# Optimization experiments

Measured on AMD Instinct MI355X. Metric: run time of the kernel, lower is better.

The kernel has to match this reference:

```python
import jax, jax.numpy as jnp
import numpy as np
import math

B, T, C = 2, 2048, 2048
NH, L = 16, 128  # n_head, LCompression


def setup_inputs() -> dict:
    key = jax.random.key(0)
    ks = jax.random.split(key, 7)
    s = 0.02
    return {
        "x": jax.random.normal(ks[0], (B, T, C), dtype=jnp.float32),
        # latent: Linear(n_embd -> LComp), stored as [in, out]
        "W_lat": jax.random.normal(ks[1], (C, L), dtype=jnp.float32) * s,
        "b_lat": jnp.zeros((L,), dtype=jnp.float32),
        # Wd: Linear(n_embd -> n_head*LComp)
        "W_d": jax.random.normal(ks[2], (C, NH * L), dtype=jnp.float32) * s,
        "b_d": jnp.zeros((NH * L,), dtype=jnp.float32),
        # c_proj: Linear(n_head*LComp -> n_embd)
        "W_proj": jax.random.normal(ks[3], (NH * L, C), dtype=jnp.float32) * s,
        "b_proj": jnp.zeros((C,), dtype=jnp.float32),
    }


def reference(x, W_lat, b_lat, W_d, b_d, W_proj, b_proj):
    Bx, Tx, Cx = x.shape
    # shared low-rank latent, used as both K and V (identical across heads)
    k = x @ W_lat + b_lat                                   # [B,T,L]
    q = (x @ W_d + b_d).reshape(Bx, Tx, NH, L)              # [B,T,H,L]
    q = jnp.transpose(q, (0, 2, 1, 3))                      # [B,H,T,L]
    scale = 1.0 / math.sqrt(L)
    # scores against the head-shared latent (no per-head K expansion)
    att = jnp.einsum("bhtl,bsl->bhts", q, k) * scale        # [B,H,T,T]
    causal = jnp.tril(jnp.ones((Tx, Tx), dtype=bool))
    att = jnp.where(causal[None, None], att, -jnp.inf)
    att = jax.nn.softmax(att, axis=-1)
    y = jnp.einsum("bhts,bsl->bhtl", att, k)                # [B,H,T,L]
    y = jnp.transpose(y, (0, 2, 1, 3)).reshape(Bx, Tx, NH * L)
    return y @ W_proj + b_proj                              # [B,T,C]
```

## Files before the change

### kernel.cpp

```cpp
#include <hip/hip_runtime.h>
#include <hip/hip_bf16.h>

#define B_   2
#define T_   2048
#define C_   2048
#define NH_  16
#define L_   128
#define NKQ  2176
#define MTOK 4096
#define SCALE2_ 0.12753785792696073f

typedef short short8 __attribute__((ext_vector_type(8)));
typedef float f32x4  __attribute__((ext_vector_type(4)));
typedef float f32x16 __attribute__((ext_vector_type(16)));

#define GLD16(gp, lp) __builtin_amdgcn_global_load_lds(                      \
    (const __attribute__((address_space(1))) void*)(gp),                     \
    (__attribute__((address_space(3))) void*)(lp), 16, 0, 0)

__device__ __forceinline__ unsigned short f2bf(float f) {
  union { float f; unsigned u; } x; x.f = f;
  unsigned r = x.u + 0x7fffu + ((x.u >> 16) & 1u);
  return (unsigned short)(r >> 16);
}

__global__ __launch_bounds__(256) void prep_all(
    const float* __restrict__ x, const float* __restrict__ W_lat,
    const float* __restrict__ W_d, const float* __restrict__ W_proj,
    const float* __restrict__ b_lat, const float* __restrict__ b_d,
    unsigned short* __restrict__ x_bf, unsigned short* __restrict__ BtCat,
    unsigned short* __restrict__ WprojT, float* __restrict__ biascat) {
  __shared__ float tile[32][33];
  int bid = blockIdx.x;
  const int tid = threadIdx.x;

  if (bid < 8192) {
    int i = bid * 1024 + tid * 4;
    float4 v = *(const float4*)(x + i);
    ushort4 o;
    o.x = f2bf(v.x); o.y = f2bf(v.y); o.z = f2bf(v.z); o.w = f2bf(v.w);
    *(ushort4*)(x_bf + i) = o;
    return;
  }
  bid -= 8192;

  const float* W; unsigned short* Wt; int K, N; float mul; int nbx;
  if (bid < 256) {
    W = W_lat; Wt = BtCat; K = C_; N = L_; mul = 1.f; nbx = 4;
  } else if (bid < 256 + 4096) {
    bid -= 256;
    W = W_d; Wt = BtCat + (size_t)L_ * C_; K = C_; N = NH_ * L_; mul = SCALE2_; nbx = 64;
  } else if (bid < 256 + 8192) {
    bid -= 256 + 4096;
    W = W_proj; Wt = WprojT; K = NH_ * L_; N = C_; mul = 1.f; nbx = 64;
  } else {
    int i = (bid - (256 + 8192)) * 256 + tid;
    if (i < L_) biascat[i] = b_lat[i];
    else if (i < NKQ) biascat[i] = b_d[i - L_] * SCALE2_;
    return;
  }

  const int bx = (bid % nbx) * 32, by = (bid / nbx) * 32;
  const int tx = tid & 31, ty = tid >> 5;
  #pragma unroll
  for (int i2 = 0; i2 < 4; i2++)
    tile[ty + i2 * 8][tx] = W[(size_t)(by + ty + i2 * 8) * N + bx + tx];
  __syncthreads();
  #pragma unroll
  for (int i2 = 0; i2 < 4; i2++)
    Wt[(size_t)(bx + ty + i2 * 8) * K + by + tx] = f2bf(tile[tx][ty + i2 * 8] * mul);
}

__global__ void transpose_lat(const unsigned short* __restrict__ kq,
                              unsigned short* __restrict__ KlT) {
  __shared__ unsigned short tile[32][33];
  int t0 = blockIdx.x * 32, l0 = blockIdx.y * 32, b = blockIdx.z;
  int tx = threadIdx.x, ty = threadIdx.y;
  #pragma unroll
  for (int i = 0; i < 4; i++)
    tile[ty + i * 8][tx] = kq[((size_t)b * T_ + t0 + ty + i * 8) * NKQ + l0 + tx];
  __syncthreads();
  #pragma unroll
  for (int i = 0; i < 4; i++)
    KlT[((size_t)b * L_ + l0 + ty + i * 8) * T_ + t0 + tx] = tile[tx][ty + i * 8];
}

__global__ __launch_bounds__(256) void gemm_bt_bias(
    const unsigned short* __restrict__ A,
    const unsigned short* __restrict__ Bt,
    const float* __restrict__ bias,
    unsigned short* __restrict__ Cb,
    float* __restrict__ Cf,
    int M, int N, int K) {
  __shared__ __align__(16) unsigned short As[2][128 * 32];
  __shared__ __align__(16) unsigned short Bs[2][128 * 32];
  const int tid  = threadIdx.x;
  const int wave = tid >> 6, lane = tid & 63;
  const int lcol = lane & 15, quad = lane >> 4;
  const int m0 = blockIdx.x * 128, n0 = blockIdx.y * 128;
  const int wm = (wave >> 1) * 64, wn = (wave & 1) * 64;
  const int lrow = lane >> 2, lchunk = (lane & 3) * 8;
  const int rb = wave * 32;

  f32x4 acc[4][4];
  #pragma unroll
  for (int i = 0; i < 4; i++)
    #pragma unroll
    for (int j = 0; j < 4; j++) acc[i][j] = (f32x4){0.f, 0.f, 0.f, 0.f};

  const int nk = K >> 5;
  GLD16(&A [(size_t)(m0 + rb      + lrow) * K + lchunk], &As[0][ rb       * 32]);
  GLD16(&A [(size_t)(m0 + rb + 16 + lrow) * K + lchunk], &As[0][(rb + 16) * 32]);
  GLD16(&Bt[(size_t)(n0 + rb      + lrow) * K + lchunk], &Bs[0][ rb       * 32]);
  GLD16(&Bt[(size_t)(n0 + rb + 16 + lrow) * K + lchunk], &Bs[0][(rb + 16) * 32]);

  for (int kt = 0; kt < nk; ++kt) {
    const int cur = kt & 1;
    __syncthreads();

    if (kt + 1 < nk) {
      const int kc = (kt + 1) << 5;
      GLD16(&A [(size_t)(m0 + rb      + lrow) * K + kc + lchunk], &As[cur ^ 1][ rb       * 32]);
      GLD16(&A [(size_t)(m0 + rb + 16 + lrow) * K + kc + lchunk], &As[cur ^ 1][(rb + 16) * 32]);
      GLD16(&Bt[(size_t)(n0 + rb      + lrow) * K + kc + lchunk], &Bs[cur ^ 1][ rb       * 32]);
      GLD16(&Bt[(size_t)(n0 + rb + 16 + lrow) * K + kc + lchunk], &Bs[cur ^ 1][(rb + 16) * 32]);
    }

    short8 af[4], bfr[4];
    #pragma unroll
    for (int i = 0; i < 4; i++)
      af[i] = *(const short8*)&As[cur][(wm + i * 16 + lcol) * 32 + quad * 8];
    #pragma unroll
    for (int j = 0; j < 4; j++)
      bfr[j] = *(const short8*)&Bs[cur][(wn + j * 16 + lcol) * 32 + quad * 8];
    #pragma unroll
    for (int i = 0; i < 4; i++)
      #pragma unroll
      for (int j = 0; j < 4; j++)
        acc[i][j] = __builtin_amdgcn_mfma_f32_16x16x32_bf16(af[i], bfr[j], acc[i][j], 0, 0, 0);
  }

  #pragma unroll
  for (int i = 0; i < 4; i++) {
    #pragma unroll
    for (int j = 0; j < 4; j++) {
      int col = n0 + wn + j * 16 + lcol;
      float bv = bias[col];
      #pragma unroll
      for (int r = 0; r < 4; r++) {
        int row = m0 + wm + i * 16 + quad * 4 + r;
        float v = acc[i][j][r] + bv;
        if (Cf) Cf[(size_t)row * N + col] = v;
        else    Cb[(size_t)row * N + col] = f2bf(v);
      }
    }
  }
}

__global__ __launch_bounds__(256, 2) void attn_mla(
    const unsigned short* __restrict__ kq,
    const unsigned short* __restrict__ KlT,
    unsigned short* __restrict__ y) {
  __shared__ __align__(16) unsigned short Kr[2][64 * 128];
  __shared__ __align__(16) unsigned short Kt[2][128 * 64];
  __shared__ __align__(16) float ls[4][32];

  const int tid  = threadIdx.x;
  const int wave = tid >> 6, lane = tid & 63;
  const int l31 = lane & 31, hf = lane >> 5;
  const int n    = blockIdx.x;
  const int slot = n >> 8, c = n & 255;
  const int hg   = c >> 5, qi = c & 31;
  const int b    = hg >> 2;
  const int h    = (hg & 3) * 4 + wave;
  const int qt32 = slot ? qi : (63 - qi);
  const size_t rowbase = (size_t)b * T_;
  const int q0 = qt32 * 32;

  short8 qf[8];
  {
    const unsigned short* qp =
        kq + (rowbase + q0 + l31) * NKQ + L_ + h * L_ + hf * 8;
    #pragma unroll
    for (int kc = 0; kc < 8; kc++)
      qf[kc] = *(const short8*)(qp + kc * 16);
  }

  f32x16 acco[4];
  #pragma unroll
  for (int nb = 0; nb < 4; nb++)
    #pragma unroll
    for (int r = 0; r < 16; r++) acco[nb][r] = 0.f;
  float lsum = 0.f;

  const int nt = (qt32 >> 1) + 1;

  #pragma unroll
  for (int kk = 0; kk < 4; kk++) {
    int r0 = wave * 16 + kk * 4;
    int rg = r0 + (lane >> 4);
    int cl = ((lane & 15) ^ (rg & 15)) * 8;
    GLD16(kq + (rowbase + rg) * NKQ + cl, &Kr[0][r0 * 128]);
  }
  #pragma unroll
  for (int kk = 0; kk < 4; kk++) {
    int r0 = wave * 32 + kk * 8;
    int rg = r0 + (lane >> 3);
    int cl = ((lane & 7) ^ (rg & 7) ^ (((rg >> 3) & 1) << 2)) * 8;
    GLD16(KlT + ((size_t)b * L_ + rg) * T_ + cl, &Kt[0][r0 * 64]);
  }

  for (int ts = 0; ts < nt; ts++) {
    const int cur = ts & 1;
    __syncthreads();

    if (ts + 1 < nt) {
      const int s1 = (ts + 1) * 64;
      #pragma unroll
      for (int kk = 0; kk < 4; kk++) {
        int r0 = wave * 16 + kk * 4;
        int rg = r0 + (lane >> 4);
        int cl = ((lane & 15) ^ (rg & 15)) * 8;
        GLD16(kq + (rowbase + s1 + rg) * NKQ + cl, &Kr[cur ^ 1][r0 * 128]);
      }
      #pragma unroll
      for (int kk = 0; kk < 4; kk++) {
        int r0 = wave * 32 + kk * 8;
        int rg = r0 + (lane >> 3);
        int cl = ((lane & 7) ^ (rg & 7) ^ (((rg >> 3) & 1) << 2)) * 8;
        GLD16(KlT + ((size_t)b * L_ + rg) * T_ + s1 + cl, &Kt[cur ^ 1][r0 * 64]);
      }
    }

    const unsigned short* Krc = &Kr[cur][0];
    const unsigned short* Ktc = &Kt[cur][0];

    f32x16 accs[2];
    #pragma unroll
    for (int sb = 0; sb < 2; sb++)
      #pragma unroll
      for (int r = 0; r < 16; r++) accs[sb][r] = 0.f;
    __builtin_amdgcn_s_setprio(1);
    #pragma unroll
    for (int kc = 0; kc < 8; kc++)
      #pragma unroll
      for (int sb = 0; sb < 2; sb++) {
        short8 kf = *(const short8*)&Krc[(sb * 32 + l31) * 128 +
                                          (((2 * kc + hf) ^ (l31 & 15)) * 8)];
        accs[sb] = __builtin_amdgcn_mfma_f32_32x32x16_bf16(kf, qf[kc], accs[sb], 0, 0, 0);
      }
    __builtin_amdgcn_s_setprio(0);

    const bool diag = (ts == nt - 1);
    const int qg = (qt32 & 1) * 32 + l31;
    #pragma unroll
    for (int sb = 0; sb < 2; sb++)
      #pragma unroll
      for (int r = 0; r < 16; r++) {
        float v = accs[sb][r];
        int s64 = sb * 32 + (r & 3) + 8 * (r >> 2) + 4 * hf;
        if (diag && s64 > qg) v = -1e30f;
        accs[sb][r] = __builtin_amdgcn_exp2f(v);
      }

    #pragma unroll
    for (int kc = 0; kc < 4; kc++) {
      const int sb = kc >> 1;
      const int t0 = (kc & 1) * 2;
      unsigned w00, w01, w10, w11;
      asm("v_cvt_pk_bf16_f32 %0, %1, %2" : "=v"(w00)
          : "v"(accs[sb][4 * t0 + 0]), "v"(accs[sb][4 * t0 + 1]));
      asm("v_cvt_pk_bf16_f32 %0, %1, %2" : "=v"(w01)
          : "v"(accs[sb][4 * t0 + 2]), "v"(accs[sb][4 * t0 + 3]));
      asm("v_cvt_pk_bf16_f32 %0, %1, %2" : "=v"(w10)
          : "v"(accs[sb][4 * t0 + 4]), "v"(accs[sb][4 * t0 + 5]));
      asm("v_cvt_pk_bf16_f32 %0, %1, %2" : "=v"(w11)
          : "v"(accs[sb][4 * t0 + 6]), "v"(accs[sb][4 * t0 + 7]));
      asm volatile("v_permlane32_swap_b32 %0, %1" : "+v"(w00), "+v"(w10));
      asm volatile("v_permlane32_swap_b32 %0, %1" : "+v"(w01), "+v"(w11));
      union { short8 s; unsigned u[4]; } F;
      F.u[0] = w00; F.u[1] = w01; F.u[2] = w10; F.u[3] = w11;
      #pragma unroll
      for (int w = 0; w < 4; w++) {
        lsum += __uint_as_float(F.u[w] << 16);
        lsum += __uint_as_float(F.u[w] & 0xffff0000u);
      }
      __builtin_amdgcn_s_setprio(1);
      #pragma unroll
      for (int nb = 0; nb < 4; nb++) {
        int rowv = nb * 32 + l31;
        short8 vf = *(const short8*)&Ktc[rowv * 64 +
            (((2 * kc + hf) ^ (rowv & 7) ^ (((rowv >> 3) & 1) << 2)) * 8)];
        acco[nb] = __builtin_amdgcn_mfma_f32_32x32x16_bf16(F.s, vf, acco[nb], 0, 0, 0);
      }
      __builtin_amdgcn_s_setprio(0);
    }
  }

  lsum += __shfl_xor(lsum, 32, 64);
  if (lane < 32) ls[wave][l31] = 1.f / lsum;
  __syncthreads();
  f32x4 rv[4];
  #pragma unroll
  for (int t = 0; t < 4; t++)
    rv[t] = *(const f32x4*)&ls[wave][8 * t + 4 * hf];

  #pragma unroll
  for (int nb = 0; nb < 4; nb++)
    #pragma unroll
    for (int r = 0; r < 16; r++) {
      int q = q0 + (r & 3) + 8 * (r >> 2) + 4 * hf;
      int l = nb * 32 + l31;
      y[(rowbase + q) * (NH_ * L_) + h * L_ + l] =
          f2bf(acco[nb][r] * rv[r >> 2][r & 3]);
    }
}

extern "C" void kernel_launch(void* const* d_in, const int* in_sizes, int n_in,
                              void* d_out, int out_size, void* d_ws, size_t ws_size,
                              hipStream_t stream) {
  const float* x      = (const float*)d_in[0];
  const float* W_lat  = (const float*)d_in[1];
  const float* b_lat  = (const float*)d_in[2];
  const float* W_d    = (const float*)d_in[3];
  const float* b_d    = (const float*)d_in[4];
  const float* W_proj = (const float*)d_in[5];
  const float* b_proj = (const float*)d_in[6];
  float* out = (float*)d_out;

  unsigned short* x_bf   = (unsigned short*)d_ws;
  unsigned short* BtCat  = x_bf   + (size_t)MTOK * C_;
  unsigned short* WprojT = BtCat  + (size_t)NKQ * C_;
  unsigned short* kqbuf  = WprojT + (size_t)C_ * (NH_ * L_);
  unsigned short* ybuf   = kqbuf  + (size_t)MTOK * NKQ;
  unsigned short* KlT    = ybuf   + (size_t)MTOK * (NH_ * L_);
  float*          biascat = (float*)(KlT + (size_t)B_ * L_ * T_);

  prep_all<<<16649, 256, 0, stream>>>(x, W_lat, W_d, W_proj, b_lat, b_d,
                                      x_bf, BtCat, WprojT, biascat);
  gemm_bt_bias<<<dim3(MTOK / 128, NKQ / 128), 256, 0, stream>>>(
      x_bf, BtCat, biascat, kqbuf, nullptr, MTOK, NKQ, C_);
  transpose_lat<<<dim3(T_ / 32, L_ / 32, B_), dim3(32, 8), 0, stream>>>(kqbuf, KlT);
  attn_mla<<<512, 256, 0, stream>>>(kqbuf, KlT, ybuf);
  gemm_bt_bias<<<dim3(MTOK / 128, C_ / 128), 256, 0, stream>>>(
      ybuf, WprojT, b_proj, nullptr, out, MTOK, C_, C_);
}
```

Baseline: 277.5 us.

## Fuse latent transpose into GEMM epilogue and load attention K/V directly from global

The separate transpose kernel is removed. The first GEMM's epilogue now also writes the transposed latent for the blocks covering the first 128 columns. The attention kernel drops its LDS double-buffered K/V staging and barriers, and instead loads K fragments and V fragments straight from global or L2 into registers, with simple register prefetch of V. This saves a launch and the LDS synchronisation, but each wave now issues redundant global loads that were previously shared through LDS. It also raises register pressure and makes the epilogue write the transpose uncoalesced.

```diff
diff --git a/kernel.cpp b/kernel.cpp
--- a/kernel.cpp
+++ b/kernel.cpp
@@ -71,26 +71,13 @@
     Wt[(size_t)(bx + ty + i2 * 8) * K + by + tx] = f2bf(tile[tx][ty + i2 * 8] * mul);
 }
 
-__global__ void transpose_lat(const unsigned short* __restrict__ kq,
-                              unsigned short* __restrict__ KlT) {
-  __shared__ unsigned short tile[32][33];
-  int t0 = blockIdx.x * 32, l0 = blockIdx.y * 32, b = blockIdx.z;
-  int tx = threadIdx.x, ty = threadIdx.y;
-  #pragma unroll
-  for (int i = 0; i < 4; i++)
-    tile[ty + i * 8][tx] = kq[((size_t)b * T_ + t0 + ty + i * 8) * NKQ + l0 + tx];
-  __syncthreads();
-  #pragma unroll
-  for (int i = 0; i < 4; i++)
-    KlT[((size_t)b * L_ + l0 + ty + i * 8) * T_ + t0 + tx] = tile[tx][ty + i * 8];
-}
-
 __global__ __launch_bounds__(256) void gemm_bt_bias(
     const unsigned short* __restrict__ A,
     const unsigned short* __restrict__ Bt,
     const float* __restrict__ bias,
     unsigned short* __restrict__ Cb,
     float* __restrict__ Cf,
+    unsigned short* __restrict__ KlTout,
     int M, int N, int K) {
   __shared__ __align__(16) unsigned short As[2][128 * 32];
   __shared__ __align__(16) unsigned short Bs[2][128 * 32];
@@ -151,7 +138,12 @@
         int row = m0 + wm + i * 16 + quad * 4 + r;
         float v = acc[i][j][r] + bv;
         if (Cf) Cf[(size_t)row * N + col] = v;
-        else    Cb[(size_t)row * N + col] = f2bf(v);
+        else {
+          unsigned short hv = f2bf(v);
+          Cb[(size_t)row * N + col] = hv;
+          if (KlTout && n0 == 0)
+            KlTout[((size_t)(row >> 11) * L_ + col) * T_ + (row & 2047)] = hv;
+        }
       }
     }
   }
@@ -161,8 +153,6 @@
     const unsigned short* __restrict__ kq,
     const unsigned short* __restrict__ KlT,
     unsigned short* __restrict__ y) {
-  __shared__ __align__(16) unsigned short Kr[2][64 * 128];
-  __shared__ __align__(16) unsigned short Kt[2][128 * 64];
   __shared__ __align__(16) float ls[4][32];
 
   const int tid  = threadIdx.x;
@@ -186,6 +176,12 @@
       qf[kc] = *(const short8*)(qp + kc * 16);
   }
 
+  const unsigned short* kp0 = kq + (rowbase + l31) * NKQ;
+  const unsigned short* vb[4];
+  #pragma unroll
+  for (int nb = 0; nb < 4; nb++)
+    vb[nb] = KlT + ((size_t)b * L_ + nb * 32 + l31) * T_;
+
   f32x16 acco[4];
   #pragma unroll
   for (int nb = 0; nb < 4; nb++)
@@ -195,45 +191,16 @@
 
   const int nt = (qt32 >> 1) + 1;
 
-  #pragma unroll
-  for (int kk = 0; kk < 4; kk++) {
-    int r0 = wave * 16 + kk * 4;
-    int rg = r0 + (lane >> 4);
-    int cl = ((lane & 15) ^ (rg & 15)) * 8;
-    GLD16(kq + (rowbase + rg) * NKQ + cl, &Kr[0][r0 * 128]);
-  }
-  #pragma unroll
-  for (int kk = 0; kk < 4; kk++) {
-    int r0 = wave * 32 + kk * 8;
-    int rg = r0 + (lane >> 3);
-    int cl = ((lane & 7) ^ (rg & 7) ^ (((rg >> 3) & 1) << 2)) * 8;
-    GLD16(KlT + ((size_t)b * L_ + rg) * T_ + cl, &Kt[0][r0 * 64]);
-  }
-
   for (int ts = 0; ts < nt; ts++) {
-    const int cur = ts & 1;
-    __syncthreads();
-
-    if (ts + 1 < nt) {
-      const int s1 = (ts + 1) * 64;
-      #pragma unroll
-      for (int kk = 0; kk < 4; kk++) {
-        int r0 = wave * 16 + kk * 4;
-        int rg = r0 + (lane >> 4);
-        int cl = ((lane & 15) ^ (rg & 15)) * 8;
-        GLD16(kq + (rowbase + s1 + rg) * NKQ + cl, &Kr[cur ^ 1][r0 * 128]);
-      }
-      #pragma unroll
-      for (int kk = 0; kk < 4; kk++) {
-        int r0 = wave * 32 + kk * 8;
-        int rg = r0 + (lane >> 3);
-        int cl = ((lane & 7) ^ (rg & 7) ^ (((rg >> 3) & 1) << 2)) * 8;
-        GLD16(KlT + ((size_t)b * L_ + rg) * T_ + s1 + cl, &Kt[cur ^ 1][r0 * 64]);
-      }
-    }
-
-    const unsigned short* Krc = &Kr[cur][0];
-    const unsigned short* Ktc = &Kt[cur][0];
+    const int s1 = ts * 64;
+
+    short8 kf[8][2];
+    #pragma unroll
+    for (int kc = 0; kc < 8; kc++)
+      #pragma unroll
+      for (int sb = 0; sb < 2; sb++)
+        kf[kc][sb] = *(const short8*)(kp0 + (size_t)(s1 + sb * 32) * NKQ +
+                                      (2 * kc + hf) * 8);
 
     f32x16 accs[2];
     #pragma unroll
@@ -244,12 +211,14 @@
     #pragma unroll
     for (int kc = 0; kc < 8; kc++)
       #pragma unroll
-      for (int sb = 0; sb < 2; sb++) {
-        short8 kf = *(const short8*)&Krc[(sb * 32 + l31) * 128 +
-                                          (((2 * kc + hf) ^ (l31 & 15)) * 8)];
-        accs[sb] = __builtin_amdgcn_mfma_f32_32x32x16_bf16(kf, qf[kc], accs[sb], 0, 0, 0);
-      }
+      for (int sb = 0; sb < 2; sb++)
+        accs[sb] = __builtin_amdgcn_mfma_f32_32x32x16_bf16(kf[kc][sb], qf[kc], accs[sb], 0, 0, 0);
     __builtin_amdgcn_s_setprio(0);
+
+    short8 vfp[2][4];
+    #pragma unroll
+    for (int nb = 0; nb < 4; nb++)
+      vfp[0][nb] = *(const short8*)(vb[nb] + s1 + hf * 8);
 
     const bool diag = (ts == nt - 1);
     const int qg = (qt32 & 1) * 32 + l31;
@@ -265,6 +234,12 @@
 
     #pragma unroll
     for (int kc = 0; kc < 4; kc++) {
+      if (kc < 3) {
+        #pragma unroll
+        for (int nb = 0; nb < 4; nb++)
+          vfp[(kc + 1) & 1][nb] =
+              *(const short8*)(vb[nb] + s1 + (2 * (kc + 1) + hf) * 8);
+      }
       const int sb = kc >> 1;
       const int t0 = (kc & 1) * 2;
       unsigned w00, w01, w10, w11;
@@ -287,12 +262,8 @@
       }
       __builtin_amdgcn_s_setprio(1);
       #pragma unroll
-      for (int nb = 0; nb < 4; nb++) {
-        int rowv = nb * 32 + l31;
-        short8 vf = *(const short8*)&Ktc[rowv * 64 +
-            (((2 * kc + hf) ^ (rowv & 7) ^ (((rowv >> 3) & 1) << 2)) * 8)];
-        acco[nb] = __builtin_amdgcn_mfma_f32_32x32x16_bf16(F.s, vf, acco[nb], 0, 0, 0);
-      }
+      for (int nb = 0; nb < 4; nb++)
+        acco[nb] = __builtin_amdgcn_mfma_f32_32x32x16_bf16(F.s, vfp[kc & 1][nb], acco[nb], 0, 0, 0);
       __builtin_amdgcn_s_setprio(0);
     }
   }
@@ -339,9 +310,8 @@
   prep_all<<<16649, 256, 0, stream>>>(x, W_lat, W_d, W_proj, b_lat, b_d,
                                       x_bf, BtCat, WprojT, biascat);
   gemm_bt_bias<<<dim3(MTOK / 128, NKQ / 128), 256, 0, stream>>>(
-      x_bf, BtCat, biascat, kqbuf, nullptr, MTOK, NKQ, C_);
-  transpose_lat<<<dim3(T_ / 32, L_ / 32, B_), dim3(32, 8), 0, stream>>>(kqbuf, KlT);
+      x_bf, BtCat, biascat, kqbuf, nullptr, KlT, MTOK, NKQ, C_);
   attn_mla<<<512, 256, 0, stream>>>(kqbuf, KlT, ybuf);
   gemm_bt_bias<<<dim3(MTOK / 128, C_ / 128), 256, 0, stream>>>(
-      ybuf, WprojT, b_proj, nullptr, out, MTOK, C_, C_);
-}
+      ybuf, WprojT, b_proj, nullptr, out, nullptr, MTOK, C_, C_);
+}
```

After: 345.0 us. 1.24x slower.

## Fuse latent transpose into QK GEMM epilogue and remap blocks per XCD

Applied to the files above, without the earlier changes.

Drops the separate transpose_lat kernel. The first GEMM's blocks that cover columns 0..127 (the latent) now also write the transposed latent directly into KlT, which saves one launch and a round trip through global memory. The GEMM block indexing is also remapped so that consecutive M tiles land on the same XCD, which should improve L2 reuse of the shared B tiles. The transposed stores are strided and uncoalesced, and the mapping assumes gridDim.x is divisible by 8.

```diff
diff --git a/kernel.cpp b/kernel.cpp
--- a/kernel.cpp
+++ b/kernel.cpp
@@ -71,33 +71,24 @@
     Wt[(size_t)(bx + ty + i2 * 8) * K + by + tx] = f2bf(tile[tx][ty + i2 * 8] * mul);
 }
 
-__global__ void transpose_lat(const unsigned short* __restrict__ kq,
-                              unsigned short* __restrict__ KlT) {
-  __shared__ unsigned short tile[32][33];
-  int t0 = blockIdx.x * 32, l0 = blockIdx.y * 32, b = blockIdx.z;
-  int tx = threadIdx.x, ty = threadIdx.y;
-  #pragma unroll
-  for (int i = 0; i < 4; i++)
-    tile[ty + i * 8][tx] = kq[((size_t)b * T_ + t0 + ty + i * 8) * NKQ + l0 + tx];
-  __syncthreads();
-  #pragma unroll
-  for (int i = 0; i < 4; i++)
-    KlT[((size_t)b * L_ + l0 + ty + i * 8) * T_ + t0 + tx] = tile[tx][ty + i * 8];
-}
-
 __global__ __launch_bounds__(256) void gemm_bt_bias(
     const unsigned short* __restrict__ A,
     const unsigned short* __restrict__ Bt,
     const float* __restrict__ bias,
     unsigned short* __restrict__ Cb,
     float* __restrict__ Cf,
+    unsigned short* __restrict__ KlTout,
     int M, int N, int K) {
   __shared__ __align__(16) unsigned short As[2][128 * 32];
   __shared__ __align__(16) unsigned short Bs[2][128 * 32];
   const int tid  = threadIdx.x;
   const int wave = tid >> 6, lane = tid & 63;
   const int lcol = lane & 15, quad = lane >> 4;
-  const int m0 = blockIdx.x * 128, n0 = blockIdx.y * 128;
+  const int lin = blockIdx.y * gridDim.x + blockIdx.x;
+  const int xcd = lin & 7, idx = lin >> 3;
+  const int mpx = gridDim.x >> 3;
+  const int m0 = (xcd * mpx + idx % mpx) * 128;
+  const int n0 = (idx / mpx) * 128;
   const int wm = (wave >> 1) * 64, wn = (wave & 1) * 64;
   const int lrow = lane >> 2, lchunk = (lane & 3) * 8;
   const int rb = wave * 32;
@@ -151,7 +142,12 @@
         int row = m0 + wm + i * 16 + quad * 4 + r;
         float v = acc[i][j][r] + bv;
         if (Cf) Cf[(size_t)row * N + col] = v;
-        else    Cb[(size_t)row * N + col] = f2bf(v);
+        else {
+          unsigned short hv = f2bf(v);
+          Cb[(size_t)row * N + col] = hv;
+          if (KlTout && n0 == 0)
+            KlTout[((size_t)(row >> 11) * L_ + col) * T_ + (row & 2047)] = hv;
+        }
       }
     }
   }
@@ -339,9 +335,8 @@
   prep_all<<<16649, 256, 0, stream>>>(x, W_lat, W_d, W_proj, b_lat, b_d,
                                       x_bf, BtCat, WprojT, biascat);
   gemm_bt_bias<<<dim3(MTOK / 128, NKQ / 128), 256, 0, stream>>>(
-      x_bf, BtCat, biascat, kqbuf, nullptr, MTOK, NKQ, C_);
-  transpose_lat<<<dim3(T_ / 32, L_ / 32, B_), dim3(32, 8), 0, stream>>>(kqbuf, KlT);
+      x_bf, BtCat, biascat, kqbuf, nullptr, KlT, MTOK, NKQ, C_);
   attn_mla<<<512, 256, 0, stream>>>(kqbuf, KlT, ybuf);
   gemm_bt_bias<<<dim3(MTOK / 128, C_ / 128), 256, 0, stream>>>(
-      ybuf, WprojT, b_proj, nullptr, out, MTOK, C_, C_);
-}
+      ybuf, WprojT, b_proj, nullptr, out, nullptr, MTOK, C_, C_);
+}
```

After: 280.8 us, median of 2. No clear change (+1.2%).
